# Kernel tuning notes

Measured on AMD Instinct MI355X. Metric: run time of the kernel, lower is better.

The kernel has to match this reference:

```python
import jax, jax.numpy as jnp
import numpy as np

EMBED_DIM = 1024
HIDDEN_DIM = 4096
NUM_EXPERTS = 8
TOP_K = 2


def setup_inputs() -> dict:
    key = jax.random.key(0)
    ks = jax.random.split(key, 5)
    x = jax.random.normal(ks[0], (2, 2048, EMBED_DIM), dtype=jnp.float32)
    Wg = jax.random.normal(ks[1], (EMBED_DIM, NUM_EXPERTS), dtype=jnp.float32) * 0.02
    W1 = jax.random.normal(ks[2], (NUM_EXPERTS, EMBED_DIM, HIDDEN_DIM), dtype=jnp.float32) * 0.02
    W3 = jax.random.normal(ks[3], (NUM_EXPERTS, EMBED_DIM, HIDDEN_DIM), dtype=jnp.float32) * 0.02
    W2 = jax.random.normal(ks[4], (NUM_EXPERTS, HIDDEN_DIM, EMBED_DIM), dtype=jnp.float32) * 0.02
    return {"x": x, "Wg": Wg, "W1": W1, "W3": W3, "W2": W2}


def reference(x, Wg, W1, W3, W2):
    # Gate: linear projection to num_experts logits
    gate = jnp.einsum("bsd,de->bse", x, Wg)  # [B,S,E]
    top_vals, top_idx = jax.lax.top_k(gate, TOP_K)  # [B,S,K]
    sel_w = jax.nn.softmax(top_vals, axis=-1)  # softmax over top-k values
    # Scatter selected weights into dense [B,S,E] (zeros for unselected experts)
    dense_w = jnp.sum(
        jax.nn.one_hot(top_idx, NUM_EXPERTS, dtype=sel_w.dtype) * sel_w[..., None],
        axis=-2,
    )  # [B,S,E]
    # Per-expert SwiGLU FFN; weight=0 for tokens not routed to expert e,
    # so the weighted-sum form is mathematically identical to masked dispatch.
    out = jnp.zeros_like(x)
    for e in range(NUM_EXPERTS):
        h = jax.nn.swish(jnp.einsum("bsd,dh->bsh", x, W1[e])) * jnp.einsum(
            "bsd,dh->bsh", x, W3[e]
        )
        out = out + dense_w[..., e:e + 1] * jnp.einsum("bsh,hd->bsd", h, W2[e])
    return out
```

## Files before the change

kernel.cpp:

```cpp
#include <hip/hip_runtime.h>
#include <hip/hip_bf16.h>
#include <stdint.h>

#define D_EMBED 1024
#define D_HID   4096
#define N_TOK   4096
#define N_EXP   8
#define CAP     4096
#define NROWA   8448

typedef __attribute__((ext_vector_type(4))) float f32x4;
typedef __attribute__((ext_vector_type(8))) short bf16x8;

__device__ __forceinline__ unsigned short f2bf(float f) {
    unsigned int u = __builtin_bit_cast(unsigned int, f);
    u += 0x7fffu + ((u >> 16) & 1u);
    return (unsigned short)(u >> 16);
}
__device__ __forceinline__ float bf2f(unsigned short h) {
    unsigned int u = ((unsigned int)h) << 16;
    return __builtin_bit_cast(float, u);
}
__device__ __forceinline__ void gload_lds16(const void* g, void* l) {
    __builtin_amdgcn_global_load_lds(
        (const __attribute__((address_space(1))) unsigned int*)g,
        (__attribute__((address_space(3))) unsigned int*)l, 16, 0, 0);
}

__global__ __launch_bounds__(256) void pack_w13(const float* __restrict__ W1,
                                                const float* __restrict__ W3,
                                                unsigned short* __restrict__ out) {
    int idx = blockIdx.x * 256 + threadIdx.x;
    int pc = idx & 8191, s = (idx >> 13) & 127, e = idx >> 20;
    int g = pc >> 4;
    int rc = ((g >> 1) << 4) + (pc & 15);
    const float* src = (g & 1 ? W3 : W1) + (size_t)e * (D_EMBED * D_HID)
                     + (size_t)(s * 8) * D_HID + rc;
    bf16x8 o;
#pragma unroll
    for (int j = 0; j < 8; ++j) o[j] = (short)f2bf(src[(size_t)j * D_HID]);
    *reinterpret_cast<bf16x8*>(out + (size_t)e * (D_EMBED * 2 * D_HID)
                               + ((size_t)s * (2 * D_HID) + pc) * 8) = o;
}

__global__ __launch_bounds__(256) void pack_w(const float* __restrict__ W,
                                              unsigned short* __restrict__ out) {
    int idx = blockIdx.x * 256 + threadIdx.x;
    int col = idx & 1023, s = (idx >> 10) & 511, e = idx >> 19;
    const float* src = W + (size_t)e * (D_HID * D_EMBED) + (size_t)(s * 8) * D_EMBED + col;
    bf16x8 o;
#pragma unroll
    for (int j = 0; j < 8; ++j) o[j] = (short)f2bf(src[(size_t)j * D_EMBED]);
    *reinterpret_cast<bf16x8*>(out + (size_t)e * (D_HID * D_EMBED)
                               + ((size_t)s * D_EMBED + col) * 8) = o;
}

__global__ __launch_bounds__(256) void gate_kernel(const float* __restrict__ x,
                                                   const float* __restrict__ Wg,
                                                   int* __restrict__ counts,
                                                   int* __restrict__ toks,
                                                   float* __restrict__ wgts,
                                                   int* __restrict__ slots) {
    int wave = threadIdx.x >> 6;
    int lane = threadIdx.x & 63;
    int tok = blockIdx.x * 4 + wave;
    const float* xp = x + (size_t)tok * D_EMBED;
    float acc[8] = {0, 0, 0, 0, 0, 0, 0, 0};
#pragma unroll
    for (int i = 0; i < 16; ++i) {
        int d = lane + 64 * i;
        float xv = xp[d];
        f32x4 w0 = *reinterpret_cast<const f32x4*>(Wg + (size_t)d * 8);
        f32x4 w1 = *reinterpret_cast<const f32x4*>(Wg + (size_t)d * 8 + 4);
        acc[0] += xv * w0[0]; acc[1] += xv * w0[1]; acc[2] += xv * w0[2]; acc[3] += xv * w0[3];
        acc[4] += xv * w1[0]; acc[5] += xv * w1[1]; acc[6] += xv * w1[2]; acc[7] += xv * w1[3];
    }
#pragma unroll
    for (int e = 0; e < 8; ++e)
        for (int s = 32; s; s >>= 1) acc[e] += __shfl_xor(acc[e], s, 64);
    if (lane == 0) {
        int i0 = 0; float v0 = acc[0];
#pragma unroll
        for (int e = 1; e < 8; ++e) if (acc[e] > v0) { v0 = acc[e]; i0 = e; }
        int i1 = -1; float v1 = -1e30f;
#pragma unroll
        for (int e = 0; e < 8; ++e) if (e != i0 && acc[e] > v1) { v1 = acc[e]; i1 = e; }
        float ex = __expf(v1 - v0);
        float w0 = 1.0f / (1.0f + ex);
        float w1 = 1.0f - w0;
        int p0 = atomicAdd(&counts[i0], 1);
        toks[i0 * CAP + p0] = tok; wgts[i0 * CAP + p0] = w0; slots[i0 * CAP + p0] = 0;
        int p1 = atomicAdd(&counts[i1], 1);
        toks[i1 * CAP + p1] = tok; wgts[i1 * CAP + p1] = w1; slots[i1 * CAP + p1] = 1;
    }
}

__global__ __launch_bounds__(256) void build_map_kernel(const int* __restrict__ counts,
                                                        const int* __restrict__ toks,
                                                        const int* __restrict__ slots,
                                                        int* __restrict__ tok2row) {
    int i = blockIdx.x * 256 + threadIdx.x;
    int e = i >> 12, pos = i & (CAP - 1);
    if (pos >= counts[e]) return;
    int off = 0;
    for (int k = 0; k < e; ++k) off += counts[k];
    tok2row[toks[i] * 2 + slots[i]] = off + pos;
}

__global__ __launch_bounds__(256) void gather_x_kernel(
    const float* __restrict__ x, const int* __restrict__ counts,
    const int* __restrict__ toks, unsigned short* __restrict__ xg) {
    int rt = blockIdx.x;
    int e = -1, tb = 0, osum = 0, rowbase = 0, cnt = 0, off = 0;
    for (int ee = 0; ee < N_EXP; ++ee) {
        int c = counts[ee];
        int nt = (c + 63) >> 6;
        if (rt < tb + nt) { e = ee; rowbase = (rt - tb) << 6; cnt = c; off = osum; break; }
        tb += nt; osum += c;
    }
    if (e < 0) return;
    int kb = blockIdx.y;
    __shared__ unsigned short lds[64][72];
    int t = threadIdx.x;
    int r = t >> 2, ck = t & 3;
    int pos = rowbase + r;
    unsigned short tmp[16];
    if (pos < cnt) {
        int tok = toks[e * CAP + pos];
        const float* src = x + (size_t)tok * D_EMBED + kb * 64 + ck * 16;
#pragma unroll
        for (int i = 0; i < 4; ++i) {
            f32x4 v = *reinterpret_cast<const f32x4*>(src + i * 4);
#pragma unroll
            for (int j = 0; j < 4; ++j) tmp[i * 4 + j] = f2bf(v[j]);
        }
    } else {
#pragma unroll
        for (int i = 0; i < 16; ++i) tmp[i] = 0;
    }
#pragma unroll
    for (int i = 0; i < 16; ++i) lds[r][ck * 16 + i] = tmp[i];
    __syncthreads();
    int sl = t >> 5, rr = (t & 31) * 2;
#pragma unroll
    for (int w = 0; w < 2; ++w) {
        int rw = rr + w;
        if (rowbase + rw >= cnt) continue;
        bf16x8 o;
#pragma unroll
        for (int j = 0; j < 8; ++j) o[j] = (short)lds[rw][sl * 8 + j];
        *reinterpret_cast<bf16x8*>(xg + ((size_t)(kb * 8 + sl) * NROWA + off + rowbase + rw) * 8) = o;
    }
}

__global__ __launch_bounds__(512, 4) void gemm1_kernel(
    const unsigned short* __restrict__ xg,
    const unsigned short* __restrict__ wt13,
    const int* __restrict__ counts,
    const float* __restrict__ wgts,
    unsigned short* __restrict__ hp) {
    int rt = blockIdx.y;
    int e = -1, tb = 0, osum = 0, rowbase = 0, cnt = 0, off = 0;
#pragma unroll 1
    for (int ee = 0; ee < N_EXP; ++ee) {
        int c = counts[ee];
        int nt = (c + 127) >> 7;
        if (rt < tb + nt) { e = ee; rowbase = (rt - tb) << 7; cnt = c; off = osum; break; }
        tb += nt; osum += c;
    }
    if (e < 0) return;
    int colp = blockIdx.x * 256;

    __shared__ __align__(16) char lds[3][24576];

    int t = threadIdx.x, lane = t & 63, w = t >> 6;
    int wr = w >> 2, wc = w & 3;
    int q = lane >> 4, p = lane & 15;

    const size_t ASTEP = (size_t)4 * NROWA * 16;
    const size_t BSTEP = (size_t)4 * (2 * D_HID) * 16;
    const char* aS = (const char*)xg + ((size_t)(t >> 7) * NROWA + off + rowbase + (t & 127)) * 16;
    const char* bS0 = (const char*)wt13 + (size_t)e * D_EMBED * 2 * D_HID * 2
                    + ((size_t)(t >> 8) * (2 * D_HID) + colp + (t & 255)) * 16;
    const char* bS1 = bS0 + (size_t)2 * (2 * D_HID) * 16;

    int wslot = 0;
    auto STG = [&]() {
        char* L = &lds[wslot][0];
        wslot = (wslot == 2) ? 0 : wslot + 1;
        gload_lds16(aS, L + t * 16);                 aS += ASTEP;
        gload_lds16(bS0, L + 8192 + t * 16);         bS0 += BSTEP;
        gload_lds16(bS1, L + 16384 + t * 16);        bS1 += BSTEP;
    };

    f32x4 acc[4][4] = {};

    STG(); STG();
    asm volatile("s_waitcnt vmcnt(3)" ::: "memory");
    __builtin_amdgcn_s_barrier();
    asm volatile("" ::: "memory");

    int rslot = 0;
#pragma unroll 1
    for (int h = 0; h < 32; ++h) {
        const char* L = &lds[rslot][0];
        rslot = (rslot == 2) ? 0 : rslot + 1;
        if (h < 30) STG();
        bf16x8 af[4], bf[4];
#pragma unroll
        for (int m = 0; m < 4; ++m)
            af[m] = *reinterpret_cast<const bf16x8*>(L + (q * 128 + wr * 64 + m * 16 + p) * 16);
#pragma unroll
        for (int n = 0; n < 4; ++n)
            bf[n] = *reinterpret_cast<const bf16x8*>(L + 8192 + (q * 256 + wc * 64 + n * 16 + p) * 16);
        asm volatile("" ::: "memory");
        __builtin_amdgcn_s_barrier();
        __builtin_amdgcn_s_setprio(1);
#pragma unroll
        for (int n = 0; n < 2; ++n)
#pragma unroll
            for (int m = 0; m < 4; ++m)
                acc[m][n] = __builtin_amdgcn_mfma_f32_16x16x32_bf16(af[m], bf[n], acc[m][n], 0, 0, 0);
        __builtin_amdgcn_s_setprio(0);
        asm volatile("" ::: "memory");
        if (h < 30) asm volatile("s_waitcnt vmcnt(3)" ::: "memory");
        else        asm volatile("s_waitcnt vmcnt(0)" ::: "memory");
        __builtin_amdgcn_s_barrier();
        __builtin_amdgcn_s_setprio(1);
#pragma unroll
        for (int n = 2; n < 4; ++n)
#pragma unroll
            for (int m = 0; m < 4; ++m)
                acc[m][n] = __builtin_amdgcn_mfma_f32_16x16x32_bf16(af[m], bf[n], acc[m][n], 0, 0, 0);
        __builtin_amdgcn_s_setprio(0);
        asm volatile("" ::: "memory");
    }

#pragma unroll
    for (int m = 0; m < 4; ++m) {
#pragma unroll
        for (int reg = 0; reg < 4; ++reg) {
            int rl = wr * 64 + m * 16 + q * 4 + reg;
            int grow = rowbase + rl;
            if (grow >= cnt) continue;
            float wgt = wgts[e * CAP + grow];
            size_t row = (size_t)(off + grow);
#pragma unroll
            for (int np = 0; np < 2; ++np) {
                float a1 = acc[m][2 * np][reg];
                float a3 = acc[m][2 * np + 1][reg];
                float hv = (a1 / (1.0f + __expf(-a1))) * a3 * wgt;
                int rc = (blockIdx.x * 8 + wc * 2 + np) * 16 + p;
                hp[((size_t)(rc >> 3) * NROWA + row) * 8 + (rc & 7)] = f2bf(hv);
            }
        }
    }
}

__global__ __launch_bounds__(512, 4) void gemm2_kernel(
    const unsigned short* __restrict__ hp,
    const unsigned short* __restrict__ wt2,
    const int* __restrict__ counts,
    unsigned short* __restrict__ pbuf) {
    int rt = blockIdx.y;
    int e = -1, tb = 0, osum = 0, rowbase = 0, cnt = 0, off = 0;
#pragma unroll 1
    for (int ee = 0; ee < N_EXP; ++ee) {
        int c = counts[ee];
        int nt = (c + 127) >> 7;
        if (rt < tb + nt) { e = ee; rowbase = (rt - tb) << 7; cnt = c; off = osum; break; }
        tb += nt; osum += c;
    }
    if (e < 0) return;
    int colb = blockIdx.x * 256;
    int s2 = blockIdx.z;

    __shared__ __align__(16) char lds[3][24576];

    int t = threadIdx.x, lane = t & 63, w = t >> 6;
    int wr = w >> 2, wc = w & 3;
    int q = lane >> 4, p = lane & 15;

    const size_t ASTEP = (size_t)4 * NROWA * 16;
    const size_t BSTEP = (size_t)4 * D_EMBED * 16;
    const char* aS = (const char*)hp
        + ((size_t)(s2 * 128 + (t >> 7)) * NROWA + off + rowbase + (t & 127)) * 16;
    const char* bS0 = (const char*)wt2 + (size_t)e * D_HID * D_EMBED * 2
        + ((size_t)(s2 * 128 + (t >> 8)) * D_EMBED + colb + (t & 255)) * 16;
    const char* bS1 = bS0 + (size_t)2 * D_EMBED * 16;

    int wslot = 0;
    auto STG = [&]() {
        char* L = &lds[wslot][0];
        wslot = (wslot == 2) ? 0 : wslot + 1;
        gload_lds16(aS, L + t * 16);                 aS += ASTEP;
        gload_lds16(bS0, L + 8192 + t * 16);         bS0 += BSTEP;
        gload_lds16(bS1, L + 16384 + t * 16);        bS1 += BSTEP;
    };

    f32x4 acc[4][4] = {};

    STG(); STG();
    asm volatile("s_waitcnt vmcnt(3)" ::: "memory");
    __builtin_amdgcn_s_barrier();
    asm volatile("" ::: "memory");

    int rslot = 0;
#pragma unroll 1
    for (int h = 0; h < 32; ++h) {
        const char* L = &lds[rslot][0];
        rslot = (rslot == 2) ? 0 : rslot + 1;
        if (h < 30) STG();
        bf16x8 af[4], bf[4];
#pragma unroll
        for (int m = 0; m < 4; ++m)
            af[m] = *reinterpret_cast<const bf16x8*>(L + (q * 128 + wr * 64 + m * 16 + p) * 16);
#pragma unroll
        for (int n = 0; n < 4; ++n)
            bf[n] = *reinterpret_cast<const bf16x8*>(L + 8192 + (q * 256 + wc * 64 + n * 16 + p) * 16);
        asm volatile("" ::: "memory");
        __builtin_amdgcn_s_barrier();
        __builtin_amdgcn_s_setprio(1);
#pragma unroll
        for (int n = 0; n < 2; ++n)
#pragma unroll
            for (int m = 0; m < 4; ++m)
                acc[m][n] = __builtin_amdgcn_mfma_f32_16x16x32_bf16(af[m], bf[n], acc[m][n], 0, 0, 0);
        __builtin_amdgcn_s_setprio(0);
        asm volatile("" ::: "memory");
        if (h < 30) asm volatile("s_waitcnt vmcnt(3)" ::: "memory");
        else        asm volatile("s_waitcnt vmcnt(0)" ::: "memory");
        __builtin_amdgcn_s_barrier();
        __builtin_amdgcn_s_setprio(1);
#pragma unroll
        for (int n = 2; n < 4; ++n)
#pragma unroll
            for (int m = 0; m < 4; ++m)
                acc[m][n] = __builtin_amdgcn_mfma_f32_16x16x32_bf16(af[m], bf[n], acc[m][n], 0, 0, 0);
        __builtin_amdgcn_s_setprio(0);
        asm volatile("" ::: "memory");
    }

    unsigned short* pb = pbuf + (size_t)s2 * 8192 * D_EMBED;
#pragma unroll
    for (int m = 0; m < 4; ++m)
#pragma unroll
        for (int reg = 0; reg < 4; ++reg) {
            int rl = wr * 64 + m * 16 + q * 4 + reg;
            int grow = rowbase + rl;
            if (grow >= cnt) continue;
            unsigned short* dst = pb + (size_t)(off + grow) * D_EMBED + colb + wc * 64;
#pragma unroll
            for (int n = 0; n < 4; ++n) dst[n * 16 + p] = f2bf(acc[m][n][reg]);
        }
}

__global__ __launch_bounds__(256) void combine_kernel(const unsigned short* __restrict__ pbuf,
                                                      const int* __restrict__ tok2row,
                                                      float* __restrict__ out) {
    int i = blockIdx.x * 256 + threadIdx.x;
    int tok = i >> 7, c0 = (i & 127) * 8;
    int r0 = tok2row[tok * 2], r1 = tok2row[tok * 2 + 1];
    const size_t SP = (size_t)8192 * D_EMBED;
    float s[8] = {0, 0, 0, 0, 0, 0, 0, 0};
#pragma unroll
    for (int sp = 0; sp < 4; ++sp) {
        bf16x8 a = *reinterpret_cast<const bf16x8*>(pbuf + sp * SP + (size_t)r0 * D_EMBED + c0);
        bf16x8 b = *reinterpret_cast<const bf16x8*>(pbuf + sp * SP + (size_t)r1 * D_EMBED + c0);
#pragma unroll
        for (int j = 0; j < 8; ++j)
            s[j] += bf2f((unsigned short)a[j]) + bf2f((unsigned short)b[j]);
    }
    float* op = out + (size_t)tok * D_EMBED + c0;
    f32x4 lo = {s[0], s[1], s[2], s[3]}, hi = {s[4], s[5], s[6], s[7]};
    *reinterpret_cast<f32x4*>(op) = lo;
    *reinterpret_cast<f32x4*>(op + 4) = hi;
}

extern "C" void kernel_launch(void* const* d_in, const int* in_sizes, int n_in,
                              void* d_out, int out_size, void* d_ws, size_t ws_size,
                              hipStream_t stream) {
    const float* x  = (const float*)d_in[0];
    const float* Wg = (const float*)d_in[1];
    const float* W1 = (const float*)d_in[2];
    const float* W3 = (const float*)d_in[3];
    const float* W2 = (const float*)d_in[4];
    float* out = (float*)d_out;

    char* ws = (char*)d_ws;
    size_t szW = (size_t)N_EXP * D_EMBED * D_HID;
    unsigned short* wt13 = (unsigned short*)ws; ws += szW * 2 * 2;
    unsigned short* wt2  = (unsigned short*)ws; ws += szW * 2;
    unsigned short* hp   = (unsigned short*)ws; ws += (size_t)(D_HID / 8) * NROWA * 8 * 2;
    unsigned short* xg   = (unsigned short*)ws; ws += (size_t)(D_EMBED / 8) * NROWA * 8 * 2;
    int*   toks    = (int*)ws;   ws += (size_t)N_EXP * CAP * 4;
    float* wgts    = (float*)ws; ws += (size_t)N_EXP * CAP * 4;
    int*   slots   = (int*)ws;   ws += (size_t)N_EXP * CAP * 4;
    int*   tok2row = (int*)ws;   ws += (size_t)N_TOK * 2 * 4;
    int*   counts  = (int*)ws;   ws += 8 * 4;
    unsigned short* pbuf = (unsigned short*)wt13;

    hipMemsetAsync(counts, 0, 8 * sizeof(int), stream);

    pack_w13<<<32768, 256, 0, stream>>>(W1, W3, wt13);
    pack_w<<<16384, 256, 0, stream>>>(W2, wt2);
    gate_kernel<<<N_TOK / 4, 256, 0, stream>>>(x, Wg, counts, toks, wgts, slots);
    build_map_kernel<<<(N_EXP * CAP) / 256, 256, 0, stream>>>(counts, toks, slots, tok2row);
    gather_x_kernel<<<dim3(136, D_EMBED / 64), 256, 0, stream>>>(x, counts, toks, xg);
    gemm1_kernel<<<dim3(32, 72), 512, 0, stream>>>(xg, wt13, counts, wgts, hp);
    gemm2_kernel<<<dim3(4, 72, 4), 512, 0, stream>>>(hp, wt2, counts, pbuf);
    combine_kernel<<<(N_TOK * 128) / 256, 256, 0, stream>>>(pbuf, tok2row, out);
}
```

Before: 475.1 us.

## Merge pack kernels, fold map build into gather, double-buffer GEMMs, halve split-K

```diff
diff --git a/kernel.cpp b/kernel.cpp
--- a/kernel.cpp
+++ b/kernel.cpp
@@ -27,32 +27,34 @@
         (__attribute__((address_space(3))) unsigned int*)l, 16, 0, 0);
 }
 
-__global__ __launch_bounds__(256) void pack_w13(const float* __restrict__ W1,
+__global__ __launch_bounds__(256) void pack_all(const float* __restrict__ W1,
                                                 const float* __restrict__ W3,
-                                                unsigned short* __restrict__ out) {
-    int idx = blockIdx.x * 256 + threadIdx.x;
-    int pc = idx & 8191, s = (idx >> 13) & 127, e = idx >> 20;
-    int g = pc >> 4;
-    int rc = ((g >> 1) << 4) + (pc & 15);
-    const float* src = (g & 1 ? W3 : W1) + (size_t)e * (D_EMBED * D_HID)
-                     + (size_t)(s * 8) * D_HID + rc;
-    bf16x8 o;
-#pragma unroll
-    for (int j = 0; j < 8; ++j) o[j] = (short)f2bf(src[(size_t)j * D_HID]);
-    *reinterpret_cast<bf16x8*>(out + (size_t)e * (D_EMBED * 2 * D_HID)
-                               + ((size_t)s * (2 * D_HID) + pc) * 8) = o;
-}
-
-__global__ __launch_bounds__(256) void pack_w(const float* __restrict__ W,
-                                              unsigned short* __restrict__ out) {
-    int idx = blockIdx.x * 256 + threadIdx.x;
-    int col = idx & 1023, s = (idx >> 10) & 511, e = idx >> 19;
-    const float* src = W + (size_t)e * (D_HID * D_EMBED) + (size_t)(s * 8) * D_EMBED + col;
-    bf16x8 o;
-#pragma unroll
-    for (int j = 0; j < 8; ++j) o[j] = (short)f2bf(src[(size_t)j * D_EMBED]);
-    *reinterpret_cast<bf16x8*>(out + (size_t)e * (D_HID * D_EMBED)
-                               + ((size_t)s * D_EMBED + col) * 8) = o;
+                                                const float* __restrict__ W2,
+                                                unsigned short* __restrict__ wt13,
+                                                unsigned short* __restrict__ wt2) {
+    int b = blockIdx.x;
+    if (b < 32768) {
+        int idx = b * 256 + threadIdx.x;
+        int pc = idx & 8191, s = (idx >> 13) & 127, e = idx >> 20;
+        int g = pc >> 4;
+        int rc = ((g >> 1) << 4) + (pc & 15);
+        const float* src = (g & 1 ? W3 : W1) + (size_t)e * (D_EMBED * D_HID)
+                         + (size_t)(s * 8) * D_HID + rc;
+        bf16x8 o;
+#pragma unroll
+        for (int j = 0; j < 8; ++j) o[j] = (short)f2bf(src[(size_t)j * D_HID]);
+        *reinterpret_cast<bf16x8*>(wt13 + (size_t)e * (D_EMBED * 2 * D_HID)
+                                   + ((size_t)s * (2 * D_HID) + pc) * 8) = o;
+    } else {
+        int idx = (b - 32768) * 256 + threadIdx.x;
+        int col = idx & 1023, s = (idx >> 10) & 511, e = idx >> 19;
+        const float* src = W2 + (size_t)e * (D_HID * D_EMBED) + (size_t)(s * 8) * D_EMBED + col;
+        bf16x8 o;
+#pragma unroll
+        for (int j = 0; j < 8; ++j) o[j] = (short)f2bf(src[(size_t)j * D_EMBED]);
+        *reinterpret_cast<bf16x8*>(wt2 + (size_t)e * (D_HID * D_EMBED)
+                                   + ((size_t)s * D_EMBED + col) * 8) = o;
+    }
 }
 
 __global__ __launch_bounds__(256) void gate_kernel(const float* __restrict__ x,
@@ -95,21 +97,10 @@
     }
 }
 
-__global__ __launch_bounds__(256) void build_map_kernel(const int* __restrict__ counts,
-                                                        const int* __restrict__ toks,
-                                                        const int* __restrict__ slots,
-                                                        int* __restrict__ tok2row) {
-    int i = blockIdx.x * 256 + threadIdx.x;
-    int e = i >> 12, pos = i & (CAP - 1);
-    if (pos >= counts[e]) return;
-    int off = 0;
-    for (int k = 0; k < e; ++k) off += counts[k];
-    tok2row[toks[i] * 2 + slots[i]] = off + pos;
-}
-
 __global__ __launch_bounds__(256) void gather_x_kernel(
     const float* __restrict__ x, const int* __restrict__ counts,
-    const int* __restrict__ toks, unsigned short* __restrict__ xg) {
+    const int* __restrict__ toks, const int* __restrict__ slots,
+    int* __restrict__ tok2row, unsigned short* __restrict__ xg) {
     int rt = blockIdx.x;
     int e = -1, tb = 0, osum = 0, rowbase = 0, cnt = 0, off = 0;
     for (int ee = 0; ee < N_EXP; ++ee) {
@@ -120,8 +111,15 @@
     }
     if (e < 0) return;
     int kb = blockIdx.y;
+    int t = threadIdx.x;
+    if (kb == 0 && t < 64) {
+        int pos = rowbase + t;
+        if (pos < cnt) {
+            int i = e * CAP + pos;
+            tok2row[toks[i] * 2 + slots[i]] = off + pos;
+        }
+    }
     __shared__ unsigned short lds[64][72];
-    int t = threadIdx.x;
     int r = t >> 2, ck = t & 3;
     int pos = rowbase + r;
     unsigned short tmp[16];
@@ -169,9 +167,8 @@
         tb += nt; osum += c;
     }
     if (e < 0) return;
-    int colp = blockIdx.x * 256;
-
-    __shared__ __align__(16) char lds[3][24576];
+
+    __shared__ __align__(16) char lds[2][24576];
 
     int t = threadIdx.x, lane = t & 63, w = t >> 6;
     int wr = w >> 2, wc = w & 3;
@@ -181,13 +178,13 @@
     const size_t BSTEP = (size_t)4 * (2 * D_HID) * 16;
     const char* aS = (const char*)xg + ((size_t)(t >> 7) * NROWA + off + rowbase + (t & 127)) * 16;
     const char* bS0 = (const char*)wt13 + (size_t)e * D_EMBED * 2 * D_HID * 2
-                    + ((size_t)(t >> 8) * (2 * D_HID) + colp + (t & 255)) * 16;
+                    + ((size_t)(t >> 8) * (2 * D_HID) + blockIdx.x * 256 + (t & 255)) * 16;
     const char* bS1 = bS0 + (size_t)2 * (2 * D_HID) * 16;
 
     int wslot = 0;
     auto STG = [&]() {
         char* L = &lds[wslot][0];
-        wslot = (wslot == 2) ? 0 : wslot + 1;
+        wslot ^= 1;
         gload_lds16(aS, L + t * 16);                 aS += ASTEP;
         gload_lds16(bS0, L + 8192 + t * 16);         bS0 += BSTEP;
         gload_lds16(bS1, L + 16384 + t * 16);        bS1 += BSTEP;
@@ -195,17 +192,15 @@
 
     f32x4 acc[4][4] = {};
 
-    STG(); STG();
-    asm volatile("s_waitcnt vmcnt(3)" ::: "memory");
-    __builtin_amdgcn_s_barrier();
-    asm volatile("" ::: "memory");
-
-    int rslot = 0;
+    STG();
 #pragma unroll 1
     for (int h = 0; h < 32; ++h) {
-        const char* L = &lds[rslot][0];
-        rslot = (rslot == 2) ? 0 : rslot + 1;
-        if (h < 30) STG();
+        if (h < 31) STG();
+        if (h < 31) asm volatile("s_waitcnt vmcnt(3)" ::: "memory");
+        else        asm volatile("s_waitcnt vmcnt(0)" ::: "memory");
+        __builtin_amdgcn_s_barrier();
+        __builtin_amdgcn_sched_barrier(0);
+        const char* L = &lds[h & 1][0];
         bf16x8 af[4], bf[4];
 #pragma unroll
         for (int m = 0; m < 4; ++m)
@@ -213,27 +208,13 @@
 #pragma unroll
         for (int n = 0; n < 4; ++n)
             bf[n] = *reinterpret_cast<const bf16x8*>(L + 8192 + (q * 256 + wc * 64 + n * 16 + p) * 16);
-        asm volatile("" ::: "memory");
-        __builtin_amdgcn_s_barrier();
         __builtin_amdgcn_s_setprio(1);
 #pragma unroll
-        for (int n = 0; n < 2; ++n)
+        for (int n = 0; n < 4; ++n)
 #pragma unroll
             for (int m = 0; m < 4; ++m)
                 acc[m][n] = __builtin_amdgcn_mfma_f32_16x16x32_bf16(af[m], bf[n], acc[m][n], 0, 0, 0);
         __builtin_amdgcn_s_setprio(0);
-        asm volatile("" ::: "memory");
-        if (h < 30) asm volatile("s_waitcnt vmcnt(3)" ::: "memory");
-        else        asm volatile("s_waitcnt vmcnt(0)" ::: "memory");
-        __builtin_amdgcn_s_barrier();
-        __builtin_amdgcn_s_setprio(1);
-#pragma unroll
-        for (int n = 2; n < 4; ++n)
-#pragma unroll
-            for (int m = 0; m < 4; ++m)
-                acc[m][n] = __builtin_amdgcn_mfma_f32_16x16x32_bf16(af[m], bf[n], acc[m][n], 0, 0, 0);
-        __builtin_amdgcn_s_setprio(0);
-        asm volatile("" ::: "memory");
     }
 
 #pragma unroll
@@ -272,10 +253,9 @@
         tb += nt; osum += c;
     }
     if (e < 0) return;
-    int colb = blockIdx.x * 256;
     int s2 = blockIdx.z;
 
-    __shared__ __align__(16) char lds[3][24576];
+    __shared__ __align__(16) char lds[2][24576];
 
     int t = threadIdx.x, lane = t & 63, w = t >> 6;
     int wr = w >> 2, wc = w & 3;
@@ -284,15 +264,15 @@
     const size_t ASTEP = (size_t)4 * NROWA * 16;
     const size_t BSTEP = (size_t)4 * D_EMBED * 16;
     const char* aS = (const char*)hp
-        + ((size_t)(s2 * 128 + (t >> 7)) * NROWA + off + rowbase + (t & 127)) * 16;
+        + ((size_t)(s2 * 256 + (t >> 7)) * NROWA + off + rowbase + (t & 127)) * 16;
     const char* bS0 = (const char*)wt2 + (size_t)e * D_HID * D_EMBED * 2
-        + ((size_t)(s2 * 128 + (t >> 8)) * D_EMBED + colb + (t & 255)) * 16;
+        + ((size_t)(s2 * 256 + (t >> 8)) * D_EMBED + blockIdx.x * 256 + (t & 255)) * 16;
     const char* bS1 = bS0 + (size_t)2 * D_EMBED * 16;
 
     int wslot = 0;
     auto STG = [&]() {
         char* L = &lds[wslot][0];
-        wslot = (wslot == 2) ? 0 : wslot + 1;
+        wslot ^= 1;
         gload_lds16(aS, L + t * 16);                 aS += ASTEP;
         gload_lds16(bS0, L + 8192 + t * 16);         bS0 += BSTEP;
         gload_lds16(bS1, L + 16384 + t * 16);        bS1 += BSTEP;
@@ -300,17 +280,15 @@
 
     f32x4 acc[4][4] = {};
 
-    STG(); STG();
-    asm volatile("s_waitcnt vmcnt(3)" ::: "memory");
-    __builtin_amdgcn_s_barrier();
-    asm volatile("" ::: "memory");
-
-    int rslot = 0;
+    STG();
 #pragma unroll 1
-    for (int h = 0; h < 32; ++h) {
-        const char* L = &lds[rslot][0];
-        rslot = (rslot == 2) ? 0 : rslot + 1;
-        if (h < 30) STG();
+    for (int h = 0; h < 64; ++h) {
+        if (h < 63) STG();
+        if (h < 63) asm volatile("s_waitcnt vmcnt(3)" ::: "memory");
+        else        asm volatile("s_waitcnt vmcnt(0)" ::: "memory");
+        __builtin_amdgcn_s_barrier();
+        __builtin_amdgcn_sched_barrier(0);
+        const char* L = &lds[h & 1][0];
         bf16x8 af[4], bf[4];
 #pragma unroll
         for (int m = 0; m < 4; ++m)
@@ -318,27 +296,13 @@
 #pragma unroll
         for (int n = 0; n < 4; ++n)
             bf[n] = *reinterpret_cast<const bf16x8*>(L + 8192 + (q * 256 + wc * 64 + n * 16 + p) * 16);
-        asm volatile("" ::: "memory");
-        __builtin_amdgcn_s_barrier();
         __builtin_amdgcn_s_setprio(1);
 #pragma unroll
-        for (int n = 0; n < 2; ++n)
+        for (int n = 0; n < 4; ++n)
 #pragma unroll
             for (int m = 0; m < 4; ++m)
                 acc[m][n] = __builtin_amdgcn_mfma_f32_16x16x32_bf16(af[m], bf[n], acc[m][n], 0, 0, 0);
         __builtin_amdgcn_s_setprio(0);
-        asm volatile("" ::: "memory");
-        if (h < 30) asm volatile("s_waitcnt vmcnt(3)" ::: "memory");
-        else        asm volatile("s_waitcnt vmcnt(0)" ::: "memory");
-        __builtin_amdgcn_s_barrier();
-        __builtin_amdgcn_s_setprio(1);
-#pragma unroll
-        for (int n = 2; n < 4; ++n)
-#pragma unroll
-            for (int m = 0; m < 4; ++m)
-                acc[m][n] = __builtin_amdgcn_mfma_f32_16x16x32_bf16(af[m], bf[n], acc[m][n], 0, 0, 0);
-        __builtin_amdgcn_s_setprio(0);
-        asm volatile("" ::: "memory");
     }
 
     unsigned short* pb = pbuf + (size_t)s2 * 8192 * D_EMBED;
@@ -349,7 +313,7 @@
             int rl = wr * 64 + m * 16 + q * 4 + reg;
             int grow = rowbase + rl;
             if (grow >= cnt) continue;
-            unsigned short* dst = pb + (size_t)(off + grow) * D_EMBED + colb + wc * 64;
+            unsigned short* dst = pb + (size_t)(off + grow) * D_EMBED + blockIdx.x * 256 + wc * 64;
 #pragma unroll
             for (int n = 0; n < 4; ++n) dst[n * 16 + p] = f2bf(acc[m][n][reg]);
         }
@@ -364,7 +328,7 @@
     const size_t SP = (size_t)8192 * D_EMBED;
     float s[8] = {0, 0, 0, 0, 0, 0, 0, 0};
 #pragma unroll
-    for (int sp = 0; sp < 4; ++sp) {
+    for (int sp = 0; sp < 2; ++sp) {
         bf16x8 a = *reinterpret_cast<const bf16x8*>(pbuf + sp * SP + (size_t)r0 * D_EMBED + c0);
         bf16x8 b = *reinterpret_cast<const bf16x8*>(pbuf + sp * SP + (size_t)r1 * D_EMBED + c0);
 #pragma unroll
@@ -402,12 +366,10 @@
 
     hipMemsetAsync(counts, 0, 8 * sizeof(int), stream);
 
-    pack_w13<<<32768, 256, 0, stream>>>(W1, W3, wt13);
-    pack_w<<<16384, 256, 0, stream>>>(W2, wt2);
+    pack_all<<<49152, 256, 0, stream>>>(W1, W3, W2, wt13, wt2);
     gate_kernel<<<N_TOK / 4, 256, 0, stream>>>(x, Wg, counts, toks, wgts, slots);
-    build_map_kernel<<<(N_EXP * CAP) / 256, 256, 0, stream>>>(counts, toks, slots, tok2row);
-    gather_x_kernel<<<dim3(136, D_EMBED / 64), 256, 0, stream>>>(x, counts, toks, xg);
+    gather_x_kernel<<<dim3(136, D_EMBED / 64), 256, 0, stream>>>(x, counts, toks, slots, tok2row, xg);
     gemm1_kernel<<<dim3(32, 72), 512, 0, stream>>>(xg, wt13, counts, wgts, hp);
-    gemm2_kernel<<<dim3(4, 72, 4), 512, 0, stream>>>(hp, wt2, counts, pbuf);
+    gemm2_kernel<<<dim3(4, 72, 2), 512, 0, stream>>>(hp, wt2, counts, pbuf);
     combine_kernel<<<(N_TOK * 128) / 256, 256, 0, stream>>>(pbuf, tok2row, out);
 }
```

New measurement: 487.4 us. +2.6%, slower.
